# Kernel tuning notes

Hardware: AMD Instinct MI355X
Metric: run time of the kernel (lower is better)

The kernel has to match this reference:

```python
import jax, jax.numpy as jnp
import numpy as np

N = 50000        # nodes
E = 800000       # edges (before self-loops)
DIM = 96         # model dim
HEADS = 4
HEAD_DIM = DIM // HEADS  # 24
SLOPE = 0.2      # GATConv default negative_slope
EPS = 1e-5       # LayerNorm eps


def setup_inputs() -> dict:
    key = jax.random.key(0)
    ks = jax.random.split(key, 10)
    s = 0.1
    return {
        "x": jax.random.normal(ks[0], (N, DIM), jnp.float32),
        "edge_index": jax.random.randint(ks[1], (2, E), 0, N, dtype=jnp.int64),
        "W": (jax.random.normal(ks[2], (DIM, HEADS * HEAD_DIM), jnp.float32) * s),
        "att_src": (jax.random.normal(ks[3], (HEADS, HEAD_DIM), jnp.float32) * s),
        "att_dst": (jax.random.normal(ks[4], (HEADS, HEAD_DIM), jnp.float32) * s),
        "gat_bias": jnp.zeros((DIM,), jnp.float32),
        "proj_W": (jax.random.normal(ks[5], (DIM, DIM), jnp.float32) * s),
        "proj_b": jnp.zeros((DIM,), jnp.float32),
        "ln_g": jnp.ones((DIM,), jnp.float32),
        "ln_b": jnp.zeros((DIM,), jnp.float32),
    }


def _gat_layer(x, edge_index, W, att_src, att_dst, gat_bias, proj_W, proj_b, ln_g, ln_b):
    # add self-loops (PyG GATConv default add_self_loops=True)
    loop = jnp.arange(N, dtype=edge_index.dtype)
    src = jnp.concatenate([edge_index[0], loop])  # [E+N] message sources j
    dst = jnp.concatenate([edge_index[1], loop])  # [E+N] message targets i

    # shared linear transform, split into heads: [N, H, D]
    h = (x @ W).reshape(N, HEADS, HEAD_DIM)
    a_src = jnp.einsum('nhd,hd->nh', h, att_src)  # [N, H]
    a_dst = jnp.einsum('nhd,hd->nh', h, att_dst)  # [N, H]

    # per-edge attention logits, leaky relu
    e = jax.nn.leaky_relu(a_src[src] + a_dst[dst], SLOPE)  # [E+N, H]

    # segment softmax over incoming edges of each destination node
    m = jax.ops.segment_max(e, dst, num_segments=N)        # [N, H]
    e = jnp.exp(e - m[dst])
    denom = jax.ops.segment_sum(e, dst, num_segments=N)    # [N, H] (>0: self-loops)
    alpha = e / denom[dst]                                 # [E+N, H]

    # weighted scatter-aggregate of source features
    out = jax.ops.segment_sum(alpha[:, :, None] * h[src], dst, num_segments=N)
    out = out.reshape(N, HEADS * HEAD_DIM) + gat_bias      # concat heads + bias

    # trailing proj + residual + LayerNorm (dropout inactive at eval)
    proj = out @ proj_W.T + proj_b
    z = x + proj
    mu = jnp.mean(z, axis=-1, keepdims=True)
    var = jnp.mean((z - mu) ** 2, axis=-1, keepdims=True)
    return ln_g * (z - mu) / jnp.sqrt(var + EPS) + ln_b


def reference(x, edge_index, W, att_src, att_dst, gat_bias, proj_W, proj_b, ln_g, ln_b):
    return _gat_layer(x, edge_index, W, att_src, att_dst, gat_bias, proj_W, proj_b, ln_g, ln_b)
```

## Files before the change

kernel.cpp:

```cpp
#include <hip/hip_runtime.h>
#include <hip/hip_bf16.h>
#include <math.h>

#define N_NODES 50000
#define N_EDGES 800000
#define DIM 96
#define HEADS 4
#define HEAD_DIM 24
#define SLOPE 0.2f
#define LN_EPS 1e-5f

#define CH 2048
#define NCH ((N_EDGES + CH - 1) / CH)
#define NB2 ((N_NODES + 255) / 256)

#define NGRP (N_NODES / 16)
#define GRID_MM 784
#define HLP 100

typedef __attribute__((ext_vector_type(8))) short bf16x8;
typedef __attribute__((ext_vector_type(4))) float f32x4;

__device__ __forceinline__ unsigned short f2bf(float f) {
    unsigned u = __float_as_uint(f);
    u += 0x7FFFu + ((u >> 16) & 1u);
    return (unsigned short)(u >> 16);
}
__device__ __forceinline__ float bf2f(unsigned short v) {
    return __uint_as_float(((unsigned)v) << 16);
}
__device__ __forceinline__ unsigned pack2bf(float a, float b) {
    return (unsigned)f2bf(a) | ((unsigned)f2bf(b) << 16);
}

__global__ void k_prep(const float* __restrict__ W, const float* __restrict__ PW,
                       unsigned short* __restrict__ wfr, unsigned short* __restrict__ pwfr)
{
    const int i = blockIdx.x * 256 + threadIdx.x;
    if (i >= 2 * 18 * 64) return;
    const int a = i / (18 * 64);
    const int rem = i % (18 * 64);
    const int frag = rem / 64, lane = rem % 64;
    const int fb = frag / 3, kc = frag % 3;
    const int m = lane & 15, g = lane >> 4;
    unsigned short* dst = (a ? pwfr : wfr) + (size_t)(frag * 64 + lane) * 8;
    #pragma unroll
    for (int j = 0; j < 8; ++j) {
        const int k = kc * 32 + g * 8 + j, f = fb * 16 + m;
        const float v = a ? PW[f * DIM + k] : W[k * DIM + f];
        dst[j] = f2bf(v);
    }
}

__global__ __launch_bounds__(256) void k_sortA(const int* __restrict__ ei,
                                               int* __restrict__ cnt)
{
    __shared__ int h[NB2];
    const int b = blockIdx.x, t = threadIdx.x;
    for (int k = t; k < NB2; k += 256) h[k] = 0;
    __syncthreads();
    const int e0 = b * CH;
    const int e1 = (e0 + CH < N_EDGES) ? e0 + CH : N_EDGES;
    for (int e = e0 + t; e < e1; e += 256) {
        const int d = ei[N_EDGES + e];
        if ((unsigned)d < N_NODES) atomicAdd(&h[d >> 8], 1);
    }
    __syncthreads();
    for (int k = t; k < NB2; k += 256) cnt[k * NCH + b] = h[k];
}

__global__ __launch_bounds__(512) void k_sortB1(const int* __restrict__ cnt,
                                                int* __restrict__ colpre,
                                                int* __restrict__ colsum)
{
    __shared__ int s[512];
    const int k = blockIdx.x, t = threadIdx.x;
    const int v = (t < NCH) ? cnt[k * NCH + t] : 0;
    s[t] = v;
    __syncthreads();
    #pragma unroll
    for (int off = 1; off < 512; off <<= 1) {
        const int u = (t >= off) ? s[t - off] : 0;
        __syncthreads();
        s[t] += u;
        __syncthreads();
    }
    if (t < NCH) colpre[k * NCH + t] = s[t] - v;
    if (t == 511) colsum[k] = s[511];
}

__global__ __launch_bounds__(256) void k_sortB2(const int* __restrict__ colsum,
                                                int* __restrict__ bbase)
{
    __shared__ int s[256];
    const int t = threadIdx.x;
    const int v = (t < NB2) ? colsum[t] : 0;
    s[t] = v;
    __syncthreads();
    #pragma unroll
    for (int off = 1; off < 256; off <<= 1) {
        const int u = (t >= off) ? s[t - off] : 0;
        __syncthreads();
        s[t] += u;
        __syncthreads();
    }
    if (t < NB2) bbase[t] = s[t] - v;
    if (t == 255) bbase[NB2] = s[255];
}

__global__ __launch_bounds__(256) void k_sortC(const int* __restrict__ ei,
                                               const int* __restrict__ colpre,
                                               const int* __restrict__ bbase,
                                               unsigned long long* __restrict__ staged)
{
    __shared__ int lcur[NB2];
    const int b = blockIdx.x, t = threadIdx.x;
    for (int k = t; k < NB2; k += 256) lcur[k] = bbase[k] + colpre[k * NCH + b];
    __syncthreads();
    const int e0 = b * CH;
    const int e1 = (e0 + CH < N_EDGES) ? e0 + CH : N_EDGES;
    for (int e = e0 + t; e < e1; e += 256) {
        int s = ei[e];
        const int d = ei[N_EDGES + e];
        if ((unsigned)d >= N_NODES) continue;
        if ((unsigned)s >= N_NODES) s = d;
        const int pos = atomicAdd(&lcur[d >> 8], 1);
        staged[pos] = (unsigned long long)(unsigned)s |
                      ((unsigned long long)(unsigned)d << 32);
    }
}

__global__ __launch_bounds__(512) void k_sortD(
    const unsigned long long* __restrict__ staged, const int* __restrict__ bbase,
    int* __restrict__ offsets, int* __restrict__ ssrc)
{
    __shared__ int hist[256];
    __shared__ int sc[256];
    const int k = blockIdx.x, t = threadIdx.x;
    const int first = k << 8;
    const int nn = (first + 256 < N_NODES) ? 256 : N_NODES - first;
    const int rs = bbase[k], re = bbase[k + 1];
    if (t < 256) hist[t] = 0;
    __syncthreads();
    for (int i = rs + t; i < re; i += 512) {
        const int d = (int)(staged[i] >> 32);
        atomicAdd(&hist[d - first], 1);
    }
    __syncthreads();
    if (t < 256) sc[t] = hist[t];
    __syncthreads();
    #pragma unroll
    for (int off = 1; off < 256; off <<= 1) {
        int u = 0;
        if (t < 256 && t >= off) u = sc[t - off];
        __syncthreads();
        if (t < 256) sc[t] += u;
        __syncthreads();
    }
    int mycur = 0;
    if (t < 256) {
        mycur = rs + sc[t] - hist[t];
        if (t < nn) offsets[first + t] = mycur;
    }
    if (k == 0 && t == 0) offsets[N_NODES] = bbase[NB2];
    __syncthreads();
    if (t < 256) hist[t] = mycur;
    __syncthreads();
    for (int i = rs + t; i < re; i += 512) {
        const unsigned long long pk = staged[i];
        const int s = (int)(pk & 0xffffffffu);
        const int d = (int)(pk >> 32);
        const int pos = atomicAdd(&hist[d - first], 1);
        ssrc[pos] = s;
    }
}

__global__ __launch_bounds__(256) void k_transform(
    const float* __restrict__ x, const unsigned short* __restrict__ wfr,
    const float* __restrict__ attS, const float* __restrict__ attD,
    unsigned short* __restrict__ hb, float* __restrict__ asrc,
    float* __restrict__ adst)
{
    __shared__ float hl[4][16][HLP];
    const int tid = threadIdx.x, wv = tid >> 6, l = tid & 63;
    const int m = l & 15, g = l >> 4;

    bf16x8 wf[6][3];
    #pragma unroll
    for (int fb = 0; fb < 6; ++fb)
        #pragma unroll
        for (int kc = 0; kc < 3; ++kc)
            wf[fb][kc] = *(const bf16x8*)&wfr[(size_t)((fb * 3 + kc) * 64 + l) * 8];

    float (*h)[HLP] = hl[wv];

    for (int grp = blockIdx.x * 4 + wv; grp < NGRP; grp += gridDim.x * 4) {
        const int n0 = grp * 16;
        f32x4 acc[6];
        #pragma unroll
        for (int fb = 0; fb < 6; ++fb)
            #pragma unroll
            for (int e = 0; e < 4; ++e) acc[fb][e] = 0.f;

        #pragma unroll
        for (int kc = 0; kc < 3; ++kc) {
            const float* xp = x + (size_t)(n0 + m) * DIM + kc * 32 + g * 8;
            const float4 xa = *(const float4*)xp;
            const float4 xb = *(const float4*)(xp + 4);
            uint4 au;
            au.x = pack2bf(xa.x, xa.y); au.y = pack2bf(xa.z, xa.w);
            au.z = pack2bf(xb.x, xb.y); au.w = pack2bf(xb.z, xb.w);
            const bf16x8 af = *(const bf16x8*)&au;
            #pragma unroll
            for (int fb = 0; fb < 6; ++fb)
                acc[fb] = __builtin_amdgcn_mfma_f32_16x16x32_bf16(af, wf[fb][kc], acc[fb], 0, 0, 0);
        }
        #pragma unroll
        for (int fb = 0; fb < 6; ++fb)
            #pragma unroll
            for (int r = 0; r < 4; ++r)
                h[g * 4 + r][fb * 16 + m] = acc[fb][r];

        {
            const int nd = l >> 2, hd = l & 3;
            const float* hr = &h[nd][hd * HEAD_DIM];
            const float* as_ = attS + hd * HEAD_DIM;
            const float* ad_ = attD + hd * HEAD_DIM;
            float s = 0.f, dd = 0.f;
            #pragma unroll
            for (int kk = 0; kk < HEAD_DIM; ++kk) {
                const float hv = hr[kk];
                s += hv * as_[kk];
                dd += hv * ad_[kk];
            }
            asrc[n0 * HEADS + l] = s;
            adst[n0 * HEADS + l] = dd;
        }
        #pragma unroll
        for (int c = l; c < 192; c += 64) {
            const int n = c / 12, q = c % 12;
            const float4 lo = *(const float4*)&h[n][q * 8];
            const float4 hi = *(const float4*)&h[n][q * 8 + 4];
            uint4 hv;
            hv.x = pack2bf(lo.x, lo.y); hv.y = pack2bf(lo.z, lo.w);
            hv.z = pack2bf(hi.x, hi.y); hv.w = pack2bf(hi.z, hi.w);
            *(uint4*)&hb[(size_t)(n0 + n) * DIM + q * 8] = hv;
        }
    }
}

__global__ __launch_bounds__(256) void k_aggregate(
    const int* __restrict__ offsets, const int* __restrict__ ssrc,
    const unsigned short* __restrict__ hb, const float* __restrict__ asrc,
    const float* __restrict__ adst, const float* __restrict__ gb,
    unsigned short* __restrict__ gbuf)
{
    const int wid  = (blockIdx.x * 256 + threadIdx.x) >> 6;
    const int lane = threadIdx.x & 63;
    if (wid >= N_NODES) return;
    const int d = wid;
    const int lp = (lane < 48) ? lane : 47;
    const int f0 = lp * 2;
    const int hd = f0 / HEAD_DIM;

    const int rs = offsets[d], re = offsets[d + 1];
    const int deg = re - rs;
    const int sv = (lane < deg) ? ssrc[rs + lane] : 0;
    const float adw = adst[d * HEADS + hd];

    float acc0, acc1, ds;
    {
        const unsigned int hp = *(const unsigned int*)&hb[(size_t)d * DIM + f0];
        float l0 = asrc[d * HEADS + hd] + adw;
        l0 = (l0 > 0.f) ? l0 : SLOPE * l0;
        const float w = __expf(l0);
        acc0 = w * bf2f((unsigned short)(hp & 0xffffu));
        acc1 = w * bf2f((unsigned short)(hp >> 16));
        ds = w;
    }

#define SRCJ(j) (((j) < 64) ? __shfl(sv, (j)) : ssrc[rs + (j)])
#define ISSUE(hreg, areg, j) do { \
        const int s_ = SRCJ(j); \
        hreg = *(const unsigned int*)&hb[(size_t)s_ * DIM + f0]; \
        areg = asrc[s_ * HEADS + hd]; } while (0)
#define CONSUME(hreg, areg) do { \
        float l_ = (areg) + adw; l_ = (l_ > 0.f) ? l_ : SLOPE * l_; \
        const float w_ = __expf(l_); \
        acc0 += w_ * bf2f((unsigned short)((hreg) & 0xffffu)); \
        acc1 += w_ * bf2f((unsigned short)((hreg) >> 16)); \
        ds += w_; } while (0)

    int j = 0;
    if (deg >= 8) {
        unsigned p0, p1, p2, p3, p4, p5, p6, p7;
        float    q0, q1, q2, q3, q4, q5, q6, q7;
        ISSUE(p0, q0, 0); ISSUE(p1, q1, 1); ISSUE(p2, q2, 2); ISSUE(p3, q3, 3);
        ISSUE(p4, q4, 4); ISSUE(p5, q5, 5); ISSUE(p6, q6, 6); ISSUE(p7, q7, 7);
        for (; j + 16 <= deg; j += 8) {
            CONSUME(p0, q0); ISSUE(p0, q0, j + 8);
            CONSUME(p1, q1); ISSUE(p1, q1, j + 9);
            CONSUME(p2, q2); ISSUE(p2, q2, j + 10);
            CONSUME(p3, q3); ISSUE(p3, q3, j + 11);
            CONSUME(p4, q4); ISSUE(p4, q4, j + 12);
            CONSUME(p5, q5); ISSUE(p5, q5, j + 13);
            CONSUME(p6, q6); ISSUE(p6, q6, j + 14);
            CONSUME(p7, q7); ISSUE(p7, q7, j + 15);
        }
        CONSUME(p0, q0); CONSUME(p1, q1); CONSUME(p2, q2); CONSUME(p3, q3);
        CONSUME(p4, q4); CONSUME(p5, q5); CONSUME(p6, q6); CONSUME(p7, q7);
        j += 8;
    }
    if (j + 4 <= deg) {
        unsigned pa, pb_, pc, pd;
        float    qa, qb, qc, qd;
        ISSUE(pa, qa, j); ISSUE(pb_, qb, j + 1); ISSUE(pc, qc, j + 2); ISSUE(pd, qd, j + 3);
        CONSUME(pa, qa); CONSUME(pb_, qb); CONSUME(pc, qc); CONSUME(pd, qd);
        j += 4;
    }
    for (; j < deg; ++j) {
        unsigned hh; float aa;
        ISSUE(hh, aa, j); CONSUME(hh, aa);
    }
#undef SRCJ
#undef ISSUE
#undef CONSUME

    if (lane < 48) {
        const float inv = 1.f / ds;
        const float o0 = acc0 * inv + gb[f0];
        const float o1 = acc1 * inv + gb[f0 + 1];
        *(unsigned*)&gbuf[(size_t)d * DIM + f0] = pack2bf(o0, o1);
    }
}

__global__ __launch_bounds__(256) void k_finalize(
    const float* __restrict__ x, const unsigned short* __restrict__ pwfr,
    const float* __restrict__ pb, const float* __restrict__ lng,
    const float* __restrict__ lnb, const unsigned short* __restrict__ gbuf,
    float* __restrict__ out)
{
    const int tid = threadIdx.x, wv = tid >> 6, l = tid & 63;
    const int m = l & 15, g = l >> 4;

    bf16x8 wf[6][3];
    #pragma unroll
    for (int fb = 0; fb < 6; ++fb)
        #pragma unroll
        for (int kc = 0; kc < 3; ++kc)
            wf[fb][kc] = *(const bf16x8*)&pwfr[(size_t)((fb * 3 + kc) * 64 + l) * 8];

    float pbv[6], lgv[6], lbv[6];
    #pragma unroll
    for (int fb = 0; fb < 6; ++fb) {
        pbv[fb] = pb[fb * 16 + m];
        lgv[fb] = lng[fb * 16 + m];
        lbv[fb] = lnb[fb * 16 + m];
    }

    for (int grp = blockIdx.x * 4 + wv; grp < NGRP; grp += gridDim.x * 4) {
        const int n0 = grp * 16;
        f32x4 acc[6];
        #pragma unroll
        for (int fb = 0; fb < 6; ++fb)
            #pragma unroll
            for (int e = 0; e < 4; ++e) acc[fb][e] = 0.f;

        #pragma unroll
        for (int kc = 0; kc < 3; ++kc) {
            const bf16x8 af = *(const bf16x8*)&gbuf[(size_t)(n0 + m) * DIM + kc * 32 + g * 8];
            #pragma unroll
            for (int fb = 0; fb < 6; ++fb)
                acc[fb] = __builtin_amdgcn_mfma_f32_16x16x32_bf16(af, wf[fb][kc], acc[fb], 0, 0, 0);
        }

        float z[6][4];
        float s0 = 0.f, s1 = 0.f, s2 = 0.f, s3 = 0.f;
        float q0 = 0.f, q1 = 0.f, q2 = 0.f, q3 = 0.f;
        #pragma unroll
        for (int fb = 0; fb < 6; ++fb) {
            #pragma unroll
            for (int r = 0; r < 4; ++r) {
                const float zv = acc[fb][r] + pbv[fb] +
                    x[(size_t)(n0 + g * 4 + r) * DIM + fb * 16 + m];
                z[fb][r] = zv;
                if (r == 0) { s0 += zv; q0 += zv * zv; }
                else if (r == 1) { s1 += zv; q1 += zv * zv; }
                else if (r == 2) { s2 += zv; q2 += zv * zv; }
                else { s3 += zv; q3 += zv * zv; }
            }
        }
        #pragma unroll
        for (int mask = 1; mask < 16; mask <<= 1) {
            s0 += __shfl_xor(s0, mask); q0 += __shfl_xor(q0, mask);
            s1 += __shfl_xor(s1, mask); q1 += __shfl_xor(q1, mask);
            s2 += __shfl_xor(s2, mask); q2 += __shfl_xor(q2, mask);
            s3 += __shfl_xor(s3, mask); q3 += __shfl_xor(q3, mask);
        }
        float mu[4], iv[4];
        mu[0] = s0 * (1.f / DIM); iv[0] = rsqrtf(q0 * (1.f / DIM) - mu[0] * mu[0] + LN_EPS);
        mu[1] = s1 * (1.f / DIM); iv[1] = rsqrtf(q1 * (1.f / DIM) - mu[1] * mu[1] + LN_EPS);
        mu[2] = s2 * (1.f / DIM); iv[2] = rsqrtf(q2 * (1.f / DIM) - mu[2] * mu[2] + LN_EPS);
        mu[3] = s3 * (1.f / DIM); iv[3] = rsqrtf(q3 * (1.f / DIM) - mu[3] * mu[3] + LN_EPS);

        #pragma unroll
        for (int fb = 0; fb < 6; ++fb)
            #pragma unroll
            for (int r = 0; r < 4; ++r)
                out[(size_t)(n0 + g * 4 + r) * DIM + fb * 16 + m] =
                    lgv[fb] * (z[fb][r] - mu[r]) * iv[r] + lbv[fb];
    }
}

extern "C" void kernel_launch(void* const* d_in, const int* in_sizes, int n_in,
                              void* d_out, int out_size, void* d_ws, size_t ws_size,
                              hipStream_t stream)
{
    const float* x    = (const float*)d_in[0];
    const int*   ei   = (const int*)d_in[1];
    const float* W    = (const float*)d_in[2];
    const float* attS = (const float*)d_in[3];
    const float* attD = (const float*)d_in[4];
    const float* gb   = (const float*)d_in[5];
    const float* PW   = (const float*)d_in[6];
    const float* pb   = (const float*)d_in[7];
    const float* lng  = (const float*)d_in[8];
    const float* lnb  = (const float*)d_in[9];
    float* out = (float*)d_out;

    char* ws = (char*)d_ws;
    unsigned long long* staged = (unsigned long long*)ws;
    float* asrc    = (float*)(staged + N_EDGES);
    float* adst    = asrc + N_NODES * HEADS;
    unsigned short* hb    = (unsigned short*)(adst + N_NODES * HEADS);
    unsigned short* gbuf  = hb + (size_t)N_NODES * DIM;
    unsigned short* wfrag = gbuf + (size_t)N_NODES * DIM;
    unsigned short* pwfrag= wfrag + 18 * 64 * 8;
    int*   cnt     = (int*)(pwfrag + 18 * 64 * 8);
    int*   colpre  = cnt + NB2 * NCH;
    int*   colsum  = colpre + NB2 * NCH;
    int*   bbase   = colsum + NB2;
    int*   offsets = bbase + NB2 + 1;
    int*   ssrc    = offsets + N_NODES + 1;

    k_prep     <<<9, 256, 0, stream>>>(W, PW, wfrag, pwfrag);
    k_sortA    <<<NCH, 256, 0, stream>>>(ei, cnt);
    k_sortB1   <<<NB2, 512, 0, stream>>>(cnt, colpre, colsum);
    k_sortB2   <<<1, 256, 0, stream>>>(colsum, bbase);
    k_sortC    <<<NCH, 256, 0, stream>>>(ei, colpre, bbase, staged);
    k_sortD    <<<NB2, 512, 0, stream>>>(staged, bbase, offsets, ssrc);
    k_transform<<<GRID_MM, 256, 0, stream>>>(x, wfrag, attS, attD, hb, asrc, adst);
    k_aggregate<<<(N_NODES * 64 + 255) / 256, 256, 0, stream>>>(offsets, ssrc, hb, asrc, adst, gb, gbuf);
    k_finalize <<<GRID_MM, 256, 0, stream>>>(x, pwfrag, pb, lng, lnb, gbuf, out);
}
```

Measured before the change: 107.2 us.

## Fuse weight prep into sort, pack staged edges, precompute attention weights in LDS

Folds the bf16 weight-fragment prep into the first sort kernel, which removes one launch. Packs the staged edge records into 32 bits (16-bit source, 8-bit local destination) instead of 64, halving that scratch traffic. In aggregation, each lane computes the four per-head exp attention weights for one incoming edge once and stores them in LDS. The gather loop then reads a weight instead of redoing the asrc load, leaky-relu and exp per feature lane. Edges past the first 64 fall back to the old path, and the 16-bit source packing relies on the node count staying below 65536.

```diff
diff --git a/kernel.cpp b/kernel.cpp
--- a/kernel.cpp
+++ b/kernel.cpp
@@ -33,28 +33,26 @@
     return (unsigned)f2bf(a) | ((unsigned)f2bf(b) << 16);
 }
 
-__global__ void k_prep(const float* __restrict__ W, const float* __restrict__ PW,
-                       unsigned short* __restrict__ wfr, unsigned short* __restrict__ pwfr)
-{
-    const int i = blockIdx.x * 256 + threadIdx.x;
-    if (i >= 2 * 18 * 64) return;
-    const int a = i / (18 * 64);
-    const int rem = i % (18 * 64);
-    const int frag = rem / 64, lane = rem % 64;
-    const int fb = frag / 3, kc = frag % 3;
-    const int m = lane & 15, g = lane >> 4;
-    unsigned short* dst = (a ? pwfr : wfr) + (size_t)(frag * 64 + lane) * 8;
-    #pragma unroll
-    for (int j = 0; j < 8; ++j) {
-        const int k = kc * 32 + g * 8 + j, f = fb * 16 + m;
-        const float v = a ? PW[f * DIM + k] : W[k * DIM + f];
-        dst[j] = f2bf(v);
-    }
-}
-
-__global__ __launch_bounds__(256) void k_sortA(const int* __restrict__ ei,
-                                               int* __restrict__ cnt)
-{
+__global__ __launch_bounds__(256) void k_sortA(
+    const int* __restrict__ ei, int* __restrict__ cnt,
+    const float* __restrict__ W, const float* __restrict__ PW,
+    unsigned short* __restrict__ wfr, unsigned short* __restrict__ pwfr)
+{
+    const int gi = blockIdx.x * 256 + threadIdx.x;
+    if (gi < 2 * 18 * 64) {
+        const int a = gi / (18 * 64);
+        const int rem = gi % (18 * 64);
+        const int frag = rem / 64, lane = rem % 64;
+        const int fb = frag / 3, kc = frag % 3;
+        const int m = lane & 15, g = lane >> 4;
+        unsigned short* dst = (a ? pwfr : wfr) + (size_t)(frag * 64 + lane) * 8;
+        #pragma unroll
+        for (int j = 0; j < 8; ++j) {
+            const int k = kc * 32 + g * 8 + j, f = fb * 16 + m;
+            const float v = a ? PW[f * DIM + k] : W[k * DIM + f];
+            dst[j] = f2bf(v);
+        }
+    }
     __shared__ int h[NB2];
     const int b = blockIdx.x, t = threadIdx.x;
     for (int k = t; k < NB2; k += 256) h[k] = 0;
@@ -111,7 +109,7 @@
 __global__ __launch_bounds__(256) void k_sortC(const int* __restrict__ ei,
                                                const int* __restrict__ colpre,
                                                const int* __restrict__ bbase,
-                                               unsigned long long* __restrict__ staged)
+                                               unsigned* __restrict__ staged)
 {
     __shared__ int lcur[NB2];
     const int b = blockIdx.x, t = threadIdx.x;
@@ -125,13 +123,12 @@
         if ((unsigned)d >= N_NODES) continue;
         if ((unsigned)s >= N_NODES) s = d;
         const int pos = atomicAdd(&lcur[d >> 8], 1);
-        staged[pos] = (unsigned long long)(unsigned)s |
-                      ((unsigned long long)(unsigned)d << 32);
+        staged[pos] = (unsigned)s | ((unsigned)(d & 255) << 16);
     }
 }
 
 __global__ __launch_bounds__(512) void k_sortD(
-    const unsigned long long* __restrict__ staged, const int* __restrict__ bbase,
+    const unsigned* __restrict__ staged, const int* __restrict__ bbase,
     int* __restrict__ offsets, int* __restrict__ ssrc)
 {
     __shared__ int hist[256];
@@ -142,10 +139,8 @@
     const int rs = bbase[k], re = bbase[k + 1];
     if (t < 256) hist[t] = 0;
     __syncthreads();
-    for (int i = rs + t; i < re; i += 512) {
-        const int d = (int)(staged[i] >> 32);
-        atomicAdd(&hist[d - first], 1);
-    }
+    for (int i = rs + t; i < re; i += 512)
+        atomicAdd(&hist[staged[i] >> 16], 1);
     __syncthreads();
     if (t < 256) sc[t] = hist[t];
     __syncthreads();
@@ -167,11 +162,9 @@
     if (t < 256) hist[t] = mycur;
     __syncthreads();
     for (int i = rs + t; i < re; i += 512) {
-        const unsigned long long pk = staged[i];
-        const int s = (int)(pk & 0xffffffffu);
-        const int d = (int)(pk >> 32);
-        const int pos = atomicAdd(&hist[d - first], 1);
-        ssrc[pos] = s;
+        const unsigned pk = staged[i];
+        const int pos = atomicAdd(&hist[pk >> 16], 1);
+        ssrc[pos] = (int)(pk & 0xffffu);
     }
 }
 
@@ -255,9 +248,11 @@
     const float* __restrict__ adst, const float* __restrict__ gb,
     unsigned short* __restrict__ gbuf)
 {
+    __shared__ float wlds[4][256];
     const int wid  = (blockIdx.x * 256 + threadIdx.x) >> 6;
     const int lane = threadIdx.x & 63;
     if (wid >= N_NODES) return;
+    const int wv = (threadIdx.x >> 6) & 3;
     const int d = wid;
     const int lp = (lane < 48) ? lane : 47;
     const int f0 = lp * 2;
@@ -265,13 +260,23 @@
 
     const int rs = offsets[d], re = offsets[d + 1];
     const int deg = re - rs;
-    const int sv = (lane < deg) ? ssrc[rs + lane] : 0;
-    const float adw = adst[d * HEADS + hd];
+    const int sv = (lane < deg) ? ssrc[rs + lane] : d;
+
+    {
+        const float4 as = *(const float4*)&asrc[sv * 4];
+        const float4 ad = *(const float4*)&adst[d * 4];
+        float l; float4 w;
+        l = as.x + ad.x; l = (l > 0.f) ? l : SLOPE * l; w.x = __expf(l);
+        l = as.y + ad.y; l = (l > 0.f) ? l : SLOPE * l; w.y = __expf(l);
+        l = as.z + ad.z; l = (l > 0.f) ? l : SLOPE * l; w.z = __expf(l);
+        l = as.w + ad.w; l = (l > 0.f) ? l : SLOPE * l; w.w = __expf(l);
+        *(float4*)&wlds[wv][lane * 4] = w;
+    }
 
     float acc0, acc1, ds;
     {
-        const unsigned int hp = *(const unsigned int*)&hb[(size_t)d * DIM + f0];
-        float l0 = asrc[d * HEADS + hd] + adw;
+        const unsigned hp = *(const unsigned*)&hb[(size_t)d * DIM + f0];
+        float l0 = asrc[d * HEADS + hd] + adst[d * HEADS + hd];
         l0 = (l0 > 0.f) ? l0 : SLOPE * l0;
         const float w = __expf(l0);
         acc0 = w * bf2f((unsigned short)(hp & 0xffffu));
@@ -279,25 +284,23 @@
         ds = w;
     }
 
-#define SRCJ(j) (((j) < 64) ? __shfl(sv, (j)) : ssrc[rs + (j)])
-#define ISSUE(hreg, areg, j) do { \
-        const int s_ = SRCJ(j); \
-        hreg = *(const unsigned int*)&hb[(size_t)s_ * DIM + f0]; \
-        areg = asrc[s_ * HEADS + hd]; } while (0)
-#define CONSUME(hreg, areg) do { \
-        float l_ = (areg) + adw; l_ = (l_ > 0.f) ? l_ : SLOPE * l_; \
-        const float w_ = __expf(l_); \
-        acc0 += w_ * bf2f((unsigned short)((hreg) & 0xffffu)); \
-        acc1 += w_ * bf2f((unsigned short)((hreg) >> 16)); \
-        ds += w_; } while (0)
-
+#define ISSUE(hreg, wreg, j) do { \
+        const int s_ = __shfl(sv, (j)); \
+        hreg = *(const unsigned*)&hb[(size_t)s_ * DIM + f0]; \
+        wreg = wlds[wv][(j) * 4 + hd]; } while (0)
+#define CONSUME(hreg, wreg) do { \
+        acc0 += (wreg) * bf2f((unsigned short)((hreg) & 0xffffu)); \
+        acc1 += (wreg) * bf2f((unsigned short)((hreg) >> 16)); \
+        ds += (wreg); } while (0)
+
+    const int nd = (deg < 64) ? deg : 64;
     int j = 0;
-    if (deg >= 8) {
+    if (nd >= 8) {
         unsigned p0, p1, p2, p3, p4, p5, p6, p7;
         float    q0, q1, q2, q3, q4, q5, q6, q7;
         ISSUE(p0, q0, 0); ISSUE(p1, q1, 1); ISSUE(p2, q2, 2); ISSUE(p3, q3, 3);
         ISSUE(p4, q4, 4); ISSUE(p5, q5, 5); ISSUE(p6, q6, 6); ISSUE(p7, q7, 7);
-        for (; j + 16 <= deg; j += 8) {
+        for (; j + 16 <= nd; j += 8) {
             CONSUME(p0, q0); ISSUE(p0, q0, j + 8);
             CONSUME(p1, q1); ISSUE(p1, q1, j + 9);
             CONSUME(p2, q2); ISSUE(p2, q2, j + 10);
@@ -311,20 +314,29 @@
         CONSUME(p4, q4); CONSUME(p5, q5); CONSUME(p6, q6); CONSUME(p7, q7);
         j += 8;
     }
-    if (j + 4 <= deg) {
+    if (j + 4 <= nd) {
         unsigned pa, pb_, pc, pd;
         float    qa, qb, qc, qd;
         ISSUE(pa, qa, j); ISSUE(pb_, qb, j + 1); ISSUE(pc, qc, j + 2); ISSUE(pd, qd, j + 3);
         CONSUME(pa, qa); CONSUME(pb_, qb); CONSUME(pc, qc); CONSUME(pd, qd);
         j += 4;
     }
-    for (; j < deg; ++j) {
-        unsigned hh; float aa;
-        ISSUE(hh, aa, j); CONSUME(hh, aa);
-    }
-#undef SRCJ
+    for (; j < nd; ++j) {
+        unsigned hh; float ww;
+        ISSUE(hh, ww, j); CONSUME(hh, ww);
+    }
 #undef ISSUE
 #undef CONSUME
+    for (j = 64; j < deg; ++j) {
+        const int s_ = ssrc[rs + j];
+        const unsigned hh = *(const unsigned*)&hb[(size_t)s_ * DIM + f0];
+        float l_ = asrc[s_ * HEADS + hd] + adst[d * HEADS + hd];
+        l_ = (l_ > 0.f) ? l_ : SLOPE * l_;
+        const float w_ = __expf(l_);
+        acc0 += w_ * bf2f((unsigned short)(hh & 0xffffu));
+        acc1 += w_ * bf2f((unsigned short)(hh >> 16));
+        ds += w_;
+    }
 
     if (lane < 48) {
         const float inv = 1.f / ds;
@@ -429,7 +441,7 @@
     float* out = (float*)d_out;
 
     char* ws = (char*)d_ws;
-    unsigned long long* staged = (unsigned long long*)ws;
+    unsigned* staged = (unsigned*)ws;
     float* asrc    = (float*)(staged + N_EDGES);
     float* adst    = asrc + N_NODES * HEADS;
     unsigned short* hb    = (unsigned short*)(adst + N_NODES * HEADS);
@@ -443,8 +455,7 @@
     int*   offsets = bbase + NB2 + 1;
     int*   ssrc    = offsets + N_NODES + 1;
 
-    k_prep     <<<9, 256, 0, stream>>>(W, PW, wfrag, pwfrag);
-    k_sortA    <<<NCH, 256, 0, stream>>>(ei, cnt);
+    k_sortA    <<<NCH, 256, 0, stream>>>(ei, cnt, W, PW, wfrag, pwfrag);
     k_sortB1   <<<NB2, 512, 0, stream>>>(cnt, colpre, colsum);
     k_sortB2   <<<1, 256, 0, stream>>>(colsum, bbase);
     k_sortC    <<<NCH, 256, 0, stream>>>(ei, colpre, bbase, staged);
```

Result: faster. 87.35 us, median of 2 (-18.5%).
